# Kernel tuning notes

Measured on AMD Instinct MI355X. Metric: run time of the kernel, lower is better.

Reference implementation:

```python
import jax, jax.numpy as jnp
import numpy as np

EMBED_DIM = 1024
NUM_HEADS = 16
HEAD_DIM = EMBED_DIM // NUM_HEADS


def setup_inputs() -> dict:
    key = jax.random.key(0)
    ks = jax.random.split(key, 9)
    bs, seq_len = 4, 2048
    s = 1.0 / np.sqrt(EMBED_DIM)
    return {
        "x": jax.random.normal(ks[0], (bs, seq_len, EMBED_DIM), jnp.float32),
        "wq": jax.random.uniform(ks[1], (EMBED_DIM, EMBED_DIM), jnp.float32, -s, s),
        "bq": jax.random.uniform(ks[2], (EMBED_DIM,), jnp.float32, -s, s),
        "wk": jax.random.uniform(ks[3], (EMBED_DIM, EMBED_DIM), jnp.float32, -s, s),
        "bk": jax.random.uniform(ks[4], (EMBED_DIM,), jnp.float32, -s, s),
        "wv": jax.random.uniform(ks[5], (EMBED_DIM, EMBED_DIM), jnp.float32, -s, s),
        "bv": jax.random.uniform(ks[6], (EMBED_DIM,), jnp.float32, -s, s),
        "wo": jax.random.uniform(ks[7], (EMBED_DIM, EMBED_DIM), jnp.float32, -s, s),
        "bo": jax.random.uniform(ks[8], (EMBED_DIM,), jnp.float32, -s, s),
    }


def reference(x, wq, bq, wk, bk, wv, bv, wo, bo):
    bs, seq_len, _ = x.shape
    # projections (torch Linear: y = x @ W.T + b; here w stored as [out,in])
    q = x @ wq.T + bq
    k = x @ wk.T + bk
    v = x @ wv.T + bv
    # split heads -> (bs, heads, seq, head_dim)
    def split(t):
        return t.reshape(bs, seq_len, NUM_HEADS, HEAD_DIM).transpose(0, 2, 1, 3)
    q, k, v = split(q), split(k), split(v)
    scale = 1.0 / jnp.sqrt(jnp.asarray(HEAD_DIM, jnp.float32))
    scores = jnp.einsum("bhqd,bhkd->bhqk", q, k) * scale
    attn = jax.nn.softmax(scores, axis=-1)
    out = jnp.einsum("bhqk,bhkd->bhqd", attn, v)
    out = out.transpose(0, 2, 1, 3).reshape(bs, seq_len, EMBED_DIM)
    return out @ wo.T + bo
```

## Files before the change

### kernel.cpp

```cpp
#include <hip/hip_runtime.h>
#include <stdint.h>

#define SEQ 2048
#define BSZ 4
#define NH 16
#define HD 64
#define EMB 1024
#define NT (SEQ / 64)
#define QSCALE 0.1803368801111f

using bf16x8 = __attribute__((ext_vector_type(8))) __bf16;
using u16x8  = __attribute__((ext_vector_type(8))) unsigned short;
using u32x4  = __attribute__((ext_vector_type(4))) uint32_t;
using f32x4  = __attribute__((ext_vector_type(4))) float;
using f32x16 = __attribute__((ext_vector_type(16))) float;

__device__ __forceinline__ float exp2v(float x) { return __builtin_amdgcn_exp2f(x); }

__device__ __forceinline__ unsigned short f2bf(float f) {
    union { float f; uint32_t u; } v; v.f = f;
    uint32_t r = v.u + 0x7fffu + ((v.u >> 16) & 1u);
    return (unsigned short)(r >> 16);
}

__device__ __forceinline__ uint32_t cvtpk(float lo, float hi) {
    uint32_t r;
    asm("v_cvt_pk_bf16_f32 %0, %1, %2" : "=v"(r) : "v"(lo), "v"(hi));
    return r;
}
__device__ __forceinline__ void plswap(uint32_t& a, uint32_t& b) {
    asm volatile("v_permlane32_swap_b32 %0, %1" : "+v"(a), "+v"(b));
}

__device__ __forceinline__ void gload16(void* lds, const void* g) {
    __builtin_amdgcn_global_load_lds(
        (const __attribute__((address_space(1))) void*)g,
        (__attribute__((address_space(3))) void*)lds, 16, 0, 0);
}

__global__ void cast_kernel(const float* __restrict__ s, unsigned short* __restrict__ d, int n) {
    int i = (blockIdx.x * blockDim.x + threadIdx.x) * 4;
    if (i + 3 >= n) {
        for (int j = 0; j < 4 && i + j < n; ++j) d[i + j] = f2bf(s[i + j]);
        return;
    }
    float4 v = *(const float4*)(s + i);
    ushort4 o;
    o.x = f2bf(v.x); o.y = f2bf(v.y); o.z = f2bf(v.z); o.w = f2bf(v.w);
    *(ushort4*)(d + i) = o;
}

template <int MODE>
__global__ __launch_bounds__(256, 2)
void gemm_bt(const unsigned short* __restrict__ A,
             const unsigned short* __restrict__ Bw,
             const float* __restrict__ b0, const float* __restrict__ b1,
             const float* __restrict__ b2,
             void* __restrict__ C0, void* __restrict__ C1, void* __restrict__ C2,
             int M, int N, int Kd) {
    __shared__ unsigned short As[128][64];
    __shared__ unsigned short Bs[128][64];

    const int t    = threadIdx.x;
    const int lane = t & 63;
    const int wid  = t >> 6;
    const int g    = lane >> 4;
    const int lr   = lane & 15;
    const int wm   = wid >> 1, wn = wid & 1;
    const int m0   = blockIdx.x * 128, n0 = blockIdx.y * 128;
    const int srow = lane >> 3;
    const int scol = (lane & 7) * 8;

    f32x4 acc[4][4];
    const f32x4 zero = {0.f, 0.f, 0.f, 0.f};
#pragma unroll
    for (int i = 0; i < 4; ++i)
#pragma unroll
        for (int j = 0; j < 4; ++j) acc[i][j] = zero;

    for (int kt = 0; kt < Kd; kt += 64) {
#pragma unroll
        for (int p = 0; p < 4; ++p) {
            int rowA = wid * 32 + p * 8;
            gload16(&As[rowA][0], A  + (size_t)(m0 + rowA + srow) * Kd + kt + scol);
            gload16(&Bs[rowA][0], Bw + (size_t)(n0 + rowA + srow) * Kd + kt + scol);
        }
        __syncthreads();
#pragma unroll
        for (int ks = 0; ks < 2; ++ks) {
            bf16x8 af[4], bfr[4];
#pragma unroll
            for (int m = 0; m < 4; ++m)
                af[m] = *(const bf16x8*)&As[wm * 64 + m * 16 + lr][ks * 32 + g * 8];
#pragma unroll
            for (int n = 0; n < 4; ++n)
                bfr[n] = *(const bf16x8*)&Bs[wn * 64 + n * 16 + lr][ks * 32 + g * 8];
#pragma unroll
            for (int m = 0; m < 4; ++m)
#pragma unroll
                for (int n = 0; n < 4; ++n)
                    acc[m][n] = __builtin_amdgcn_mfma_f32_16x16x32_bf16(af[m], bfr[n], acc[m][n], 0, 0, 0);
        }
        __syncthreads();
    }

    const float* bias;
    unsigned short* Cw = nullptr;
    float* Cf = nullptr;
    float scl = 1.0f;
    int nl;
    if (MODE == 2) {
        int seg = n0 >> 10;
        bias = seg == 0 ? b0 : (seg == 1 ? b1 : b2);
        Cw = (unsigned short*)(seg == 0 ? C0 : (seg == 1 ? C1 : C2));
        scl = seg == 0 ? QSCALE : 1.0f;
        nl = n0 & 1023;
    } else {
        bias = b0; Cf = (float*)C0; nl = n0;
    }
#pragma unroll
    for (int n = 0; n < 4; ++n) {
        int colL = nl + wn * 64 + n * 16 + lr;
        float bv = bias[colL];
#pragma unroll
        for (int m = 0; m < 4; ++m) {
            int rowg = m0 + wm * 64 + m * 16 + g * 4;
#pragma unroll
            for (int r = 0; r < 4; ++r) {
                float val = (acc[m][n][r] + bv) * scl;
                if (MODE == 2)
                    Cw[(size_t)(rowg + r) * EMB + colL] = f2bf(val);
                else
                    Cf[(size_t)(rowg + r) * EMB + colL] = val;
            }
        }
    }
}

template <int M>
__device__ __forceinline__ void xr(uint32_t d[4], int i) {
    uint32_t o[4];
#pragma unroll
    for (int k = 0; k < 4; ++k) o[k] = (uint32_t)__shfl_xor((int)d[k], M);
    if (M == 1) {
        bool hi = (i & 1) != 0;
#pragma unroll
        for (int k = 0; k < 4; ++k)
            d[k] = hi ? ((d[k] & 0xffff0000u) | (o[k] >> 16))
                      : ((d[k] & 0x0000ffffu) | (o[k] << 16));
    } else {
        const int mb = M >> 1;
        bool hi = (i & M) != 0;
#pragma unroll
        for (int jd = 0; jd < 4; ++jd) {
            bool jdhi = (jd & mb) != 0;
            d[jd] = (jdhi != hi) ? o[jd ^ mb] : d[jd];
        }
    }
}

__global__ __launch_bounds__(512, 4)
void flash_attn(const unsigned short* __restrict__ Q,
                const unsigned short* __restrict__ K,
                const unsigned short* __restrict__ V,
                unsigned short* __restrict__ O) {
    __shared__ unsigned char KsB[2][64 * 128];
    __shared__ unsigned char VtB[2][64 * 128];

    const int nwg  = gridDim.x * gridDim.y * gridDim.z;
    const int cpx  = nwg >> 3;
    const int bid0 = (blockIdx.z * gridDim.y + blockIdx.y) * gridDim.x + blockIdx.x;
    const int bid  = (bid0 % 8) * cpx + (bid0 / 8);
    const int bx   = bid & (gridDim.x - 1);
    const int h    = (bid >> 3) & 15;
    const int b    = bid >> 7;

    const int t    = threadIdx.x;
    const int wid  = t >> 6;
    const int lane = t & 63;
    const int l31  = lane & 31;
    const int hi   = lane >> 5;
    const int hi16 = hi << 4;
    const int sw   = (l31 & 7) << 4;
    const int il   = lane & 7;
    const int qbase = bx * 256 + wid * 32;
    const size_t rowbase = (size_t)b * SEQ;
    const unsigned short* Kh = K + rowbase * EMB + h * HD;
    const unsigned short* Vh = V + rowbase * EMB + h * HD;

    bf16x8 qf[4];
#pragma unroll
    for (int db = 0; db < 4; ++db)
        qf[db] = *(const bf16x8*)(Q + (rowbase + qbase + l31) * EMB + h * HD + db * 16 + hi * 8);

    f32x16 o0, o1;
#pragma unroll
    for (int r = 0; r < 16; ++r) { o0[r] = 0.f; o1[r] = 0.f; }
    float me = -1e30f, lsum = 0.f;

    const int krow = t >> 3;
    const int kcol = (t & 7) << 3;
    const int vcb  = (lane >> 3) << 3;
    u16x8 kreg, vreg;
    auto load_tile = [&](int kt) {
        kreg = *(const u16x8*)(Kh + (size_t)(kt * 64 + krow) * EMB + kcol);
        vreg = *(const u16x8*)(Vh + (size_t)(kt * 64 + wid * 8 + il) * EMB + vcb);
    };
    load_tile(0);

    for (int kt = 0; kt < NT; ++kt) {
        unsigned char* Ks = KsB[kt & 1];
        unsigned char* Vt = VtB[kt & 1];

        uint32_t tv[4];
        {
            u32x4 w = __builtin_bit_cast(u32x4, vreg);
#pragma unroll
            for (int k = 0; k < 4; ++k) tv[k] = w[k];
            xr<4>(tv, il);
            xr<2>(tv, il);
            xr<1>(tv, il);
        }
        *(u16x8*)(Ks + krow * 128 + (((t & 7) << 4) ^ ((krow & 7) << 4))) = kreg;
        *(u32x4*)(Vt + lane * 128 + ((wid << 4) ^ ((lane & 7) << 4))) = *(u32x4*)tv;

        if (kt + 1 < NT) load_tile(kt + 1);

        __syncthreads();

        f32x16 s0, s1;
#pragma unroll
        for (int r = 0; r < 16; ++r) { s0[r] = 0.f; s1[r] = 0.f; }
        __builtin_amdgcn_s_setprio(1);
#pragma unroll
        for (int db = 0; db < 4; ++db) {
            bf16x8 kf0 = *(const bf16x8*)(Ks + l31 * 128        + ((db * 32 + hi16) ^ sw));
            bf16x8 kf1 = *(const bf16x8*)(Ks + (l31 + 32) * 128 + ((db * 32 + hi16) ^ sw));
            s0 = __builtin_amdgcn_mfma_f32_32x32x16_bf16(kf0, qf[db], s0, 0, 0, 0);
            s1 = __builtin_amdgcn_mfma_f32_32x32x16_bf16(kf1, qf[db], s1, 0, 0, 0);
        }
        __builtin_amdgcn_s_setprio(0);

        float pm = fmaxf(s0[0], s0[1]);
#pragma unroll
        for (int r = 2; r < 16; ++r) pm = fmaxf(pm, s0[r]);
#pragma unroll
        for (int r = 0; r < 16; ++r) pm = fmaxf(pm, s1[r]);
        pm = fmaxf(pm, __shfl_xor(pm, 32));

        if (!__all(pm - me <= 8.0f)) {
            float mn = fmaxf(me, pm);
            float al = exp2v(me - mn);
            me = mn;
            lsum *= al;
#pragma unroll
            for (int r = 0; r < 16; ++r) {
                int addr = hi16 + (((r & 3) + 8 * (r >> 2)) << 2);
                float ar = __int_as_float(
                    __builtin_amdgcn_ds_bpermute(addr, __float_as_int(al)));
                o0[r] *= ar; o1[r] *= ar;
            }
        }

        float rs = 0.f;
#pragma unroll
        for (int r = 0; r < 16; ++r) { s0[r] = exp2v(s0[r] - me); rs += s0[r]; }
#pragma unroll
        for (int r = 0; r < 16; ++r) { s1[r] = exp2v(s1[r] - me); rs += s1[r]; }
        rs += __shfl_xor(rs, 32);
        lsum += rs;

        bf16x8 pa[4];
#pragma unroll
        for (int kb = 0; kb < 2; ++kb) {
            uint32_t dw[8];
#pragma unroll
            for (int i = 0; i < 8; ++i)
                dw[i] = kb == 0 ? cvtpk(s0[2 * i], s0[2 * i + 1])
                                : cvtpk(s1[2 * i], s1[2 * i + 1]);
            plswap(dw[0], dw[2]); plswap(dw[1], dw[3]);
            plswap(dw[4], dw[6]); plswap(dw[5], dw[7]);
            u32x4 w0 = {dw[0], dw[1], dw[2], dw[3]};
            u32x4 w1 = {dw[4], dw[5], dw[6], dw[7]};
            pa[kb * 2]     = __builtin_bit_cast(bf16x8, w0);
            pa[kb * 2 + 1] = __builtin_bit_cast(bf16x8, w1);
        }

        __builtin_amdgcn_s_setprio(1);
#pragma unroll
        for (int kk = 0; kk < 4; ++kk) {
            bf16x8 vf0 = *(const bf16x8*)(Vt + l31 * 128        + ((kk * 32 + hi16) ^ sw));
            bf16x8 vf1 = *(const bf16x8*)(Vt + (l31 + 32) * 128 + ((kk * 32 + hi16) ^ sw));
            o0 = __builtin_amdgcn_mfma_f32_32x32x16_bf16(pa[kk], vf0, o0, 0, 0, 0);
            o1 = __builtin_amdgcn_mfma_f32_32x32x16_bf16(pa[kk], vf1, o1, 0, 0, 0);
        }
        __builtin_amdgcn_s_setprio(0);
    }

#pragma unroll
    for (int r = 0; r < 16; ++r) {
        int addr = hi16 + (((r & 3) + 8 * (r >> 2)) << 2);
        float lr_ = __int_as_float(__builtin_amdgcn_ds_bpermute(addr, __float_as_int(lsum)));
        float inv = 1.0f / lr_;
        int q = qbase + (r & 3) + 8 * (r >> 2) + 4 * hi;
        size_t ro = (rowbase + q) * EMB + h * HD;
        O[ro + l31]      = f2bf(o0[r] * inv);
        O[ro + 32 + l31] = f2bf(o1[r] * inv);
    }
}

extern "C" void kernel_launch(void* const* d_in, const int* in_sizes, int n_in,
                              void* d_out, int out_size, void* d_ws, size_t ws_size,
                              hipStream_t stream) {
    const float* x  = (const float*)d_in[0];
    const float* wq = (const float*)d_in[1];
    const float* bq = (const float*)d_in[2];
    const float* wk = (const float*)d_in[3];
    const float* bk = (const float*)d_in[4];
    const float* wv = (const float*)d_in[5];
    const float* bv = (const float*)d_in[6];
    const float* wo = (const float*)d_in[7];
    const float* bo = (const float*)d_in[8];

    char* ws = (char*)d_ws;
    const size_t M = (size_t)BSZ * SEQ;
    unsigned short* xb    = (unsigned short*)ws;
    unsigned short* wqkvb = (unsigned short*)(ws + (size_t)16 * 1024 * 1024);
    unsigned short* wob   = (unsigned short*)(ws + (size_t)22 * 1024 * 1024);
    unsigned short* Qb    = (unsigned short*)(ws + (size_t)24 * 1024 * 1024);
    unsigned short* Kb    = Qb + M * EMB;
    unsigned short* Vb    = Kb + M * EMB;

    const int nX = (int)(M * EMB);
    cast_kernel<<<nX / 1024, 256, 0, stream>>>(x, xb, nX);
    cast_kernel<<<1024, 256, 0, stream>>>(wq, wqkvb,                 EMB * EMB);
    cast_kernel<<<1024, 256, 0, stream>>>(wk, wqkvb + 1024 * 1024,   EMB * EMB);
    cast_kernel<<<1024, 256, 0, stream>>>(wv, wqkvb + 2 * 1024 * 1024, EMB * EMB);
    cast_kernel<<<1024, 256, 0, stream>>>(wo, wob, EMB * EMB);

    gemm_bt<2><<<dim3(64, 24), 256, 0, stream>>>(xb, wqkvb, bq, bk, bv,
                                                 Qb, Kb, Vb, (int)M, 3 * EMB, EMB);

    flash_attn<<<dim3(SEQ / 256, NH, BSZ), 512, 0, stream>>>(Qb, Kb, Vb, xb);

    gemm_bt<0><<<dim3(64, 8), 256, 0, stream>>>(xb, wob, bo, nullptr, nullptr,
                                                d_out, nullptr, nullptr, (int)M, EMB, EMB);
}
```

Baseline: 221.4 us.

## Write V transposed from QKV GEMM and stream K/V tiles directly into LDS

The QKV projection epilogue now stores V in a per-head transposed layout (dim-major, sequence contiguous). This removes the in-register shuffle transpose from the attention loop. The attention kernel then loads K and V tiles straight into LDS with a gload16 helper (likely direct global-to-LDS loads), issued right after the barrier for the next tile, so the register staging and ds_write pass go away. The max reduction is also restructured into pairwise fmax chains. The transposed V store writes 4-element strided chunks, which may coalesce poorly in the GEMM epilogue, and gload16 is not visible in the shown code.

```diff
diff --git a/kernel.cpp b/kernel.cpp
--- a/kernel.cpp
+++ b/kernel.cpp
@@ -104,15 +104,37 @@
         __syncthreads();
     }
 
+    int seg = MODE == 2 ? (n0 >> 10) : 0;
+    if (MODE == 2 && seg == 2) {
+        unsigned short* CwT = (unsigned short*)C2;
+        int nl = n0 & 1023;
+#pragma unroll
+        for (int n = 0; n < 4; ++n) {
+            int colL = nl + wn * 64 + n * 16 + lr;
+            float bv = b2[colL];
+#pragma unroll
+            for (int m = 0; m < 4; ++m) {
+                int rowg = m0 + wm * 64 + m * 16 + g * 4;
+                int bb = rowg >> 11, seq = rowg & 2047;
+                ushort4 w;
+                w.x = f2bf(acc[m][n][0] + bv);
+                w.y = f2bf(acc[m][n][1] + bv);
+                w.z = f2bf(acc[m][n][2] + bv);
+                w.w = f2bf(acc[m][n][3] + bv);
+                *(ushort4*)(CwT + ((size_t)(bb * 1024 + colL)) * SEQ + seq) = w;
+            }
+        }
+        return;
+    }
+
     const float* bias;
     unsigned short* Cw = nullptr;
     float* Cf = nullptr;
     float scl = 1.0f;
     int nl;
     if (MODE == 2) {
-        int seg = n0 >> 10;
-        bias = seg == 0 ? b0 : (seg == 1 ? b1 : b2);
-        Cw = (unsigned short*)(seg == 0 ? C0 : (seg == 1 ? C1 : C2));
+        bias = seg == 0 ? b0 : b1;
+        Cw = (unsigned short*)(seg == 0 ? C0 : C1);
         scl = seg == 0 ? QSCALE : 1.0f;
         nl = n0 & 1023;
     } else {
@@ -137,32 +159,10 @@
     }
 }
 
-template <int M>
-__device__ __forceinline__ void xr(uint32_t d[4], int i) {
-    uint32_t o[4];
-#pragma unroll
-    for (int k = 0; k < 4; ++k) o[k] = (uint32_t)__shfl_xor((int)d[k], M);
-    if (M == 1) {
-        bool hi = (i & 1) != 0;
-#pragma unroll
-        for (int k = 0; k < 4; ++k)
-            d[k] = hi ? ((d[k] & 0xffff0000u) | (o[k] >> 16))
-                      : ((d[k] & 0x0000ffffu) | (o[k] << 16));
-    } else {
-        const int mb = M >> 1;
-        bool hi = (i & M) != 0;
-#pragma unroll
-        for (int jd = 0; jd < 4; ++jd) {
-            bool jdhi = (jd & mb) != 0;
-            d[jd] = (jdhi != hi) ? o[jd ^ mb] : d[jd];
-        }
-    }
-}
-
 __global__ __launch_bounds__(512, 4)
 void flash_attn(const unsigned short* __restrict__ Q,
                 const unsigned short* __restrict__ K,
-                const unsigned short* __restrict__ V,
+                const unsigned short* __restrict__ VT,
                 unsigned short* __restrict__ O) {
     __shared__ unsigned char KsB[2][64 * 128];
     __shared__ unsigned char VtB[2][64 * 128];
@@ -182,11 +182,15 @@
     const int hi   = lane >> 5;
     const int hi16 = hi << 4;
     const int sw   = (l31 & 7) << 4;
-    const int il   = lane & 7;
     const int qbase = bx * 256 + wid * 32;
     const size_t rowbase = (size_t)b * SEQ;
-    const unsigned short* Kh = K + rowbase * EMB + h * HD;
-    const unsigned short* Vh = V + rowbase * EMB + h * HD;
+    const unsigned short* Kh  = K + rowbase * EMB + h * HD;
+    const unsigned short* Vth = VT + (size_t)(b * 1024 + h * HD) * SEQ;
+
+    const int grow = t >> 3;
+    const int gc16 = (t & 7) ^ (grow & 7);
+    const unsigned short* Ksrc0 = Kh  + (size_t)grow * EMB + gc16 * 8;
+    const unsigned short* Vsrc0 = Vth + (size_t)grow * SEQ + gc16 * 8;
 
     bf16x8 qf[4];
 #pragma unroll
@@ -198,35 +202,21 @@
     for (int r = 0; r < 16; ++r) { o0[r] = 0.f; o1[r] = 0.f; }
     float me = -1e30f, lsum = 0.f;
 
-    const int krow = t >> 3;
-    const int kcol = (t & 7) << 3;
-    const int vcb  = (lane >> 3) << 3;
-    u16x8 kreg, vreg;
-    auto load_tile = [&](int kt) {
-        kreg = *(const u16x8*)(Kh + (size_t)(kt * 64 + krow) * EMB + kcol);
-        vreg = *(const u16x8*)(Vh + (size_t)(kt * 64 + wid * 8 + il) * EMB + vcb);
+    auto issue_tile = [&](int kt) {
+        unsigned char* Ks = KsB[kt & 1] + wid * 1024;
+        unsigned char* Vt = VtB[kt & 1] + wid * 1024;
+        gload16(Ks, Ksrc0 + (size_t)kt * 64 * EMB);
+        gload16(Vt, Vsrc0 + kt * 64);
     };
-    load_tile(0);
+    issue_tile(0);
 
     for (int kt = 0; kt < NT; ++kt) {
         unsigned char* Ks = KsB[kt & 1];
         unsigned char* Vt = VtB[kt & 1];
 
-        uint32_t tv[4];
-        {
-            u32x4 w = __builtin_bit_cast(u32x4, vreg);
-#pragma unroll
-            for (int k = 0; k < 4; ++k) tv[k] = w[k];
-            xr<4>(tv, il);
-            xr<2>(tv, il);
-            xr<1>(tv, il);
-        }
-        *(u16x8*)(Ks + krow * 128 + (((t & 7) << 4) ^ ((krow & 7) << 4))) = kreg;
-        *(u32x4*)(Vt + lane * 128 + ((wid << 4) ^ ((lane & 7) << 4))) = *(u32x4*)tv;
-
-        if (kt + 1 < NT) load_tile(kt + 1);
-
         __syncthreads();
+
+        if (kt + 1 < NT) issue_tile(kt + 1);
 
         f32x16 s0, s1;
 #pragma unroll
@@ -241,11 +231,12 @@
         }
         __builtin_amdgcn_s_setprio(0);
 
-        float pm = fmaxf(s0[0], s0[1]);
-#pragma unroll
-        for (int r = 2; r < 16; ++r) pm = fmaxf(pm, s0[r]);
-#pragma unroll
-        for (int r = 0; r < 16; ++r) pm = fmaxf(pm, s1[r]);
+        float pm = fmaxf(fmaxf(s0[0], s0[1]), s0[2]);
+#pragma unroll
+        for (int r = 3; r < 15; r += 2) pm = fmaxf(fmaxf(pm, s0[r]), s0[r + 1]);
+        pm = fmaxf(pm, s0[15]);
+#pragma unroll
+        for (int r = 0; r < 16; r += 2) pm = fmaxf(fmaxf(pm, s1[r]), s1[r + 1]);
         pm = fmaxf(pm, __shfl_xor(pm, 32));
 
         if (!__all(pm - me <= 8.0f)) {
@@ -329,7 +320,7 @@
     unsigned short* wob   = (unsigned short*)(ws + (size_t)22 * 1024 * 1024);
     unsigned short* Qb    = (unsigned short*)(ws + (size_t)24 * 1024 * 1024);
     unsigned short* Kb    = Qb + M * EMB;
-    unsigned short* Vb    = Kb + M * EMB;
+    unsigned short* VTb   = Kb + M * EMB;
 
     const int nX = (int)(M * EMB);
     cast_kernel<<<nX / 1024, 256, 0, stream>>>(x, xb, nX);
@@ -339,9 +330,9 @@
     cast_kernel<<<1024, 256, 0, stream>>>(wo, wob, EMB * EMB);
 
     gemm_bt<2><<<dim3(64, 24), 256, 0, stream>>>(xb, wqkvb, bq, bk, bv,
-                                                 Qb, Kb, Vb, (int)M, 3 * EMB, EMB);
-
-    flash_attn<<<dim3(SEQ / 256, NH, BSZ), 512, 0, stream>>>(Qb, Kb, Vb, xb);
+                                                 Qb, Kb, VTb, (int)M, 3 * EMB, EMB);
+
+    flash_attn<<<dim3(SEQ / 256, NH, BSZ), 512, 0, stream>>>(Qb, Kb, VTb, xb);
 
     gemm_bt<0><<<dim3(64, 8), 256, 0, stream>>>(xb, wob, bo, nullptr, nullptr,
                                                 d_out, nullptr, nullptr, (int)M, EMB, EMB);
```

Measured after the change: 204.8 us. 7.5% less time.
